# Kernel optimization log

Hardware: AMD Instinct MI355X
Metric: run time of the kernel (lower is better)

Reference implementation:

```python
import jax, jax.numpy as jnp
import numpy as np

B, T, D, V, L = 32, 512, 512, 1024, 128
BLANK = 0
NEG = -1e30  # log-domain 'minus infinity' that is fp-safe


def setup_inputs() -> dict:
    key = jax.random.key(0)
    k1, k2, k3 = jax.random.split(key, 3)
    x = jax.random.normal(k1, (B, T, D), dtype=jnp.float32)
    W = jax.random.normal(k2, (D, V), dtype=jnp.float32) / np.sqrt(D).astype(np.float32)
    b = jnp.zeros((V,), dtype=jnp.float32)
    # CTC targets must be in [1, V) (never the blank id 0)
    target = jax.random.randint(k3, (B, L), 1, V)
    input_lengths = jnp.full((B,), T, dtype=jnp.int32)
    target_lengths = jnp.full((B,), L, dtype=jnp.int32)
    return {"x": x, "W": W, "b": b, "target": target,
            "input_lengths": input_lengths, "target_lengths": target_lengths}


def _ctc_loss(log_probs, target, input_lengths, target_lengths):
    # log_probs: [T, B, V] (time-major), target: [B, L]
    Tt, Bb, _ = log_probs.shape
    Ll = target.shape[1]
    S = 2 * Ll + 1  # extended label sequence: blank,t0,blank,t1,...,blank
    ext = jnp.full((Bb, S), BLANK, dtype=target.dtype).at[:, 1::2].set(target)  # [B,S]
    ext_m2 = jnp.pad(ext, ((0, 0), (2, 0)), constant_values=BLANK)[:, :S]
    skip = (ext != BLANK) & (ext != ext_m2) & (jnp.arange(S)[None, :] >= 2)  # [B,S]

    # gather log-probs of extended labels for every time step: [T,B,S]
    lp_ext = jnp.take_along_axis(log_probs, jnp.broadcast_to(ext[None], (Tt, Bb, S)), axis=2)

    alpha0 = jnp.full((Bb, S), NEG, log_probs.dtype)
    alpha0 = alpha0.at[:, 0].set(lp_ext[0, :, 0]).at[:, 1].set(lp_ext[0, :, 1])

    def step(alpha, lp_t):
        a1 = jnp.pad(alpha, ((0, 0), (1, 0)), constant_values=NEG)[:, :S]
        a2 = jnp.pad(alpha, ((0, 0), (2, 0)), constant_values=NEG)[:, :S]
        c = jnp.logaddexp(alpha, a1)
        c = jnp.where(skip, jnp.logaddexp(c, a2), c)
        new = c + lp_t
        return new, new

    _, alphas = jax.lax.scan(step, alpha0, lp_ext[1:])
    alphas = jnp.concatenate([alpha0[None], alphas], axis=0)  # [T,B,S]

    bi = jnp.arange(Bb)
    a_last = alphas[input_lengths - 1, bi]  # [B,S] alpha at each sample's final frame
    ll = jnp.logaddexp(a_last[bi, 2 * target_lengths - 1], a_last[bi, 2 * target_lengths])
    nll = -ll  # per-sample negative log-likelihood
    # zero_infinity=True: infinite losses are zeroed
    nll = jnp.where(jnp.isinf(nll) | (nll > 1e29), 0.0, nll)
    # reduction='mean': divide each loss by its target length, then mean
    return jnp.mean(nll / jnp.maximum(target_lengths, 1).astype(nll.dtype))


def reference(x, W, b, target, input_lengths, target_lengths):
    logits = jnp.einsum('btd,dv->btv', x, W) + b  # nn.Linear
    log_probs = jax.nn.log_softmax(logits, axis=-1)  # [B,T,V]
    return _ctc_loss(jnp.transpose(log_probs, (1, 0, 2)), target, input_lengths, target_lengths)
```

## Files before the change

### kernel.cpp

```cpp
#include <hip/hip_runtime.h>
#include <cstdint>


#define SPAD 260
#define PEXT_PAD_ROWS 32
#define L2E 1.4426950408889634f
#define LN2 0.6931471805599453f

typedef short v8s __attribute__((ext_vector_type(8)));
typedef float v4f __attribute__((ext_vector_type(4)));

__device__ __forceinline__ uint32_t f2bf_bits(float f) {
  uint32_t u = __float_as_uint(f);
  return (u + 0x7FFFu + ((u >> 16) & 1u)) >> 16;
}
__device__ __forceinline__ float bf2f(uint32_t h) { return __uint_as_float(h << 16); }

__global__ void k_convert_x(const float* __restrict__ x, uint16_t* __restrict__ xb, long long n) {
  long long i = ((long long)blockIdx.x * blockDim.x + threadIdx.x) * 8;
  if (i >= n) return;
  float4 a = *(const float4*)(x + i);
  float4 b = *(const float4*)(x + i + 4);
  uint4 o;
  o.x = f2bf_bits(a.x) | (f2bf_bits(a.y) << 16);
  o.y = f2bf_bits(a.z) | (f2bf_bits(a.w) << 16);
  o.z = f2bf_bits(b.x) | (f2bf_bits(b.y) << 16);
  o.w = f2bf_bits(b.z) | (f2bf_bits(b.w) << 16);
  *(uint4*)(xb + i) = o;
}

__global__ void k_transpose_w(const float* __restrict__ W, uint16_t* __restrict__ Wt, int D, int V) {
  __shared__ float tile[32][33];
  int n0 = blockIdx.x * 32, k0 = blockIdx.y * 32;
  int tx = threadIdx.x, ty = threadIdx.y;
  #pragma unroll
  for (int i = 0; i < 32; i += 8)
    tile[ty + i][tx] = W[(size_t)(k0 + ty + i) * V + n0 + tx];
  __syncthreads();
  #pragma unroll
  for (int i = 0; i < 32; i += 8)
    Wt[(size_t)(n0 + ty + i) * D + k0 + tx] = (uint16_t)f2bf_bits(tile[tx][ty + i]);
}

template <typename CT>
__global__ __launch_bounds__(256) void k_gemm(const uint16_t* __restrict__ A,
                                              const uint16_t* __restrict__ Bt,
                                              const float* __restrict__ bias,
                                              CT* __restrict__ C, int M, int N, int K) {
  __shared__ uint16_t As[128 * 32];
  __shared__ uint16_t Bs[128 * 32];
  const int tid = threadIdx.x, lane = tid & 63, wave = tid >> 6;
  const int m0 = blockIdx.x * 128, n0 = blockIdx.y * 128;
  const int wm = wave & 1, wn = wave >> 1;
  const int frow = lane & 15, kb = lane >> 4;
  const int lr = lane >> 2, kc = lane & 3;
  v4f acc[4][4] = {};

  for (int k0 = 0; k0 < K; k0 += 32) {
    __syncthreads();
    #pragma unroll
    for (int i = 0; i < 2; i++) {
      const int r = (wave * 2 + i) * 16 + lr;
      const uint16_t* ga = A + (size_t)(m0 + r) * K + k0 + kc * 8;
      const uint16_t* gb = Bt + (size_t)(n0 + r) * K + k0 + kc * 8;
      __builtin_amdgcn_global_load_lds(
          (const __attribute__((address_space(1))) void*)ga,
          (__attribute__((address_space(3))) void*)(As + (wave * 2 + i) * 512 + lane * 8), 16, 0, 0);
      __builtin_amdgcn_global_load_lds(
          (const __attribute__((address_space(1))) void*)gb,
          (__attribute__((address_space(3))) void*)(Bs + (wave * 2 + i) * 512 + lane * 8), 16, 0, 0);
    }
    __syncthreads();

    v8s af[4], bf[4];
    #pragma unroll
    for (int i = 0; i < 4; i++)
      af[i] = *(const v8s*)(As + (wm * 64 + i * 16 + frow) * 32 + kb * 8);
    #pragma unroll
    for (int j = 0; j < 4; j++)
      bf[j] = *(const v8s*)(Bs + (wn * 64 + j * 16 + frow) * 32 + kb * 8);
    #pragma unroll
    for (int i = 0; i < 4; i++)
      #pragma unroll
      for (int j = 0; j < 4; j++)
        acc[i][j] = __builtin_amdgcn_mfma_f32_16x16x32_bf16(af[i], bf[j], acc[i][j], 0, 0, 0);
  }

  const int crow = (lane >> 4) * 4, ccol = lane & 15;
  #pragma unroll
  for (int j = 0; j < 4; j++) {
    const int n = n0 + wn * 64 + j * 16 + ccol;
    const float bv = bias[n];
    #pragma unroll
    for (int i = 0; i < 4; i++) {
      const int mb = m0 + wm * 64 + i * 16 + crow;
      #pragma unroll
      for (int r2 = 0; r2 < 4; r2++) {
        float v = acc[i][j][r2] + bv;
        if constexpr (sizeof(CT) == 2) C[(size_t)(mb + r2) * N + n] = (CT)f2bf_bits(v);
        else                           C[(size_t)(mb + r2) * N + n] = v;
      }
    }
  }
}

template <typename CT>
__global__ void k_softmax_gather(const CT* __restrict__ logits, const int* __restrict__ target,
                                 const int* __restrict__ tlen, float* __restrict__ pext,
                                 int T, int V, int L) {
  const int row = blockIdx.x * 4 + (threadIdx.x >> 6);
  const int lane = threadIdx.x & 63;
  const CT* lrow = logits + (size_t)row * V;

  float xs[16];
  int cnt = 0;
  float mx = -INFINITY;
  for (int base = 0; base < V; base += 256) {
    const int idx = base + lane * 4;
    float4 v;
    if constexpr (sizeof(CT) == 2) {
      uint2 u = *(const uint2*)((const uint16_t*)lrow + idx);
      v.x = bf2f(u.x & 0xFFFFu); v.y = bf2f(u.x >> 16);
      v.z = bf2f(u.y & 0xFFFFu); v.w = bf2f(u.y >> 16);
    } else {
      v = *(const float4*)((const float*)lrow + idx);
    }
    xs[cnt] = v.x; xs[cnt + 1] = v.y; xs[cnt + 2] = v.z; xs[cnt + 3] = v.w; cnt += 4;
    mx = fmaxf(mx, fmaxf(fmaxf(v.x, v.y), fmaxf(v.z, v.w)));
  }
  #pragma unroll
  for (int off = 32; off; off >>= 1) mx = fmaxf(mx, __shfl_xor(mx, off, 64));
  float sum = 0.f;
  #pragma unroll
  for (int q = 0; q < 16; q++) { if (q < cnt) sum += exp2f((xs[q] - mx) * L2E); }
  #pragma unroll
  for (int off = 32; off; off >>= 1) sum += __shfl_xor(sum, off, 64);
  const float lse2 = mx * L2E + log2f(sum);

  const int bidx = row / T;
  const int Lb = tlen[bidx];
  const int S = 2 * Lb + 1;
  float* prow = pext + (size_t)row * SPAD;
  for (int s = lane; s < SPAD; s += 64) {
    float p = 0.f;
    if (s < S) {
      const int lbl = (s & 1) ? target[bidx * L + ((s - 1) >> 1)] : 0;
      float lg;
      if constexpr (sizeof(CT) == 2) lg = bf2f(((const uint16_t*)lrow)[lbl]);
      else                           lg = ((const float*)lrow)[lbl];
      p = exp2f(lg * L2E - lse2);
    }
    prow[s] = p;
  }
}

__device__ __forceinline__ float wave_shr1(float x) {
  return __int_as_float(__builtin_amdgcn_update_dpp(0, __float_as_int(x), 0x138, 0xf, 0xf, true));
}
__device__ __forceinline__ float wave_max_nonneg(float x) {
  x = fmaxf(x, __int_as_float(__builtin_amdgcn_update_dpp(0, __float_as_int(x), 0x111, 0xf, 0xf, true)));
  x = fmaxf(x, __int_as_float(__builtin_amdgcn_update_dpp(0, __float_as_int(x), 0x112, 0xf, 0xf, true)));
  x = fmaxf(x, __int_as_float(__builtin_amdgcn_update_dpp(0, __float_as_int(x), 0x114, 0xf, 0xf, true)));
  x = fmaxf(x, __int_as_float(__builtin_amdgcn_update_dpp(0, __float_as_int(x), 0x118, 0xf, 0xf, true)));
  x = fmaxf(x, __int_as_float(__builtin_amdgcn_update_dpp(0, __float_as_int(x), 0x142, 0xf, 0xf, true)));
  x = fmaxf(x, __int_as_float(__builtin_amdgcn_update_dpp(0, __float_as_int(x), 0x143, 0xf, 0xf, true)));
  return __int_as_float(__builtin_amdgcn_readlane(__float_as_int(x), 63));
}

__device__ __forceinline__ void load16(float4* __restrict__ p, float* __restrict__ p4,
                                       const float* __restrict__ pb, int t0, int lane) {
  #pragma unroll
  for (int k = 0; k < 16; k++) {
    const float* row = pb + (size_t)(t0 + k) * SPAD;
    p[k] = *(const float4*)(row + (lane << 2));
    p4[k] = row[256];
  }
}

__global__ __launch_bounds__(64, 1) void k_ctc(const float* __restrict__ pext,
                                               const int* __restrict__ target,
                                               const int* __restrict__ ilen,
                                               const int* __restrict__ tlen,
                                               float* __restrict__ loss, int T, int L) {
  const int b = blockIdx.x;
  const int lane = threadIdx.x;
  const int Tb = ilen[b];
  const int Lb = tlen[b];
  const int S = 2 * Lb + 1;
  const int* tg = target + b * L;

  const int s1 = 4 * lane + 1, s3 = 4 * lane + 3;
  float sk1 = 0.f, sk3 = 0.f;
  if (s1 >= 3 && s1 < S) sk1 = (tg[(s1 - 1) >> 1] != tg[(s1 - 3) >> 1]) ? 1.f : 0.f;
  if (s3 >= 3 && s3 < S) sk3 = (tg[(s3 - 1) >> 1] != tg[(s3 - 3) >> 1]) ? 1.f : 0.f;

  const float* pb = pext + (size_t)b * T * SPAD;
  const float4 p0 = *(const float4*)(pb + (lane << 2));
  float a0 = (lane == 0) ? p0.x : 0.f;
  float a1 = (lane == 0) ? p0.y : 0.f;
  float a2 = 0.f, a3 = 0.f, a4 = 0.f;
  float log2C = 0.f;

  #define CTC_STEP(PP, P4) {                                            \
    const float pm3 = wave_shr1(a3);                                    \
    const float a255 = __int_as_float(__builtin_amdgcn_readlane(__float_as_int(a3), 63)); \
    const float n0v = (a0 + pm3) * (PP).x;                              \
    const float n1v = (a1 + a0 + sk1 * pm3) * (PP).y;                   \
    const float n2v = (a2 + a1) * (PP).z;                               \
    const float n3v = (a3 + a2 + sk3 * a1) * (PP).w;                    \
    const float n4v = (a4 + a255) * (P4);                               \
    a0 = n0v; a1 = n1v; a2 = n2v; a3 = n3v; a4 = n4v; }

  #define RENORM {                                                      \
    float m = fmaxf(fmaxf(fmaxf(a0, a1), fmaxf(a2, a3)), a4);           \
    m = wave_max_nonneg(m);                                             \
    const int e = (int)((__float_as_uint(m) >> 23) & 255u) - 127;       \
    const float scale = __uint_as_float((uint32_t)(127 - e) << 23);     \
    a0 *= scale; a1 *= scale; a2 *= scale; a3 *= scale; a4 *= scale;    \
    log2C += (float)e; }

  float4 pA[16], pB[16];
  float p4A[16], p4B[16];
  int t0 = 1;
  load16(pA, p4A, pb, t0, lane);

  while (t0 < Tb) {
    load16(pB, p4B, pb, t0 + 16, lane);
    #pragma unroll
    for (int k = 0; k < 16; k++) {
      if (t0 + k < Tb) CTC_STEP(pA[k], p4A[k]);
      if ((k & 7) == 7) RENORM;
    }
    t0 += 16;
    if (t0 >= Tb) break;
    load16(pA, p4A, pb, t0 + 16, lane);
    #pragma unroll
    for (int k = 0; k < 16; k++) {
      if (t0 + k < Tb) CTC_STEP(pB[k], p4B[k]);
      if ((k & 7) == 7) RENORM;
    }
    t0 += 16;
  }

  __shared__ float abuf[257];
  abuf[4 * lane + 0] = a0; abuf[4 * lane + 1] = a1;
  abuf[4 * lane + 2] = a2; abuf[4 * lane + 3] = a3;
  if (lane == 63) abuf[256] = a4;
  __syncthreads();
  if (lane == 0) {
    const float ssum = abuf[2 * Lb - 1] + abuf[2 * Lb];
    const float ll = (log2f(ssum) + log2C) * LN2;
    float nll = -ll;
    if (!(nll < 1e29f)) nll = 0.f;
    loss[b] = nll / (float)(Lb > 0 ? Lb : 1);
  }
}

__global__ void k_reduce(const float* __restrict__ loss, float* __restrict__ out, int B) {
  const int lane = threadIdx.x;
  float v = (lane < B) ? loss[lane] : 0.f;
  #pragma unroll
  for (int off = 32; off; off >>= 1) v += __shfl_xor(v, off, 64);
  if (lane == 0) out[0] = v / (float)B;
}

extern "C" void kernel_launch(void* const* d_in, const int* in_sizes, int n_in,
                              void* d_out, int out_size, void* d_ws, size_t ws_size,
                              hipStream_t stream) {
  const float* x      = (const float*)d_in[0];
  const float* W      = (const float*)d_in[1];
  const float* bias   = (const float*)d_in[2];
  const int*  target  = (const int*)d_in[3];
  const int*  ilen    = (const int*)d_in[4];
  const int*  tlen    = (const int*)d_in[5];

  const int B = in_sizes[4];
  const int V = in_sizes[2];
  const int D = in_sizes[1] / V;
  const int T = in_sizes[0] / (B * D);
  const int L = in_sizes[3] / B;
  const int M = B * T;

  char* ws = (char*)d_ws;
  const size_t xb_bytes = (size_t)M * D * 2;
  const size_t wt_bytes = (size_t)V * D * 2;
  const size_t pext_bytes = (size_t)(M + PEXT_PAD_ROWS) * SPAD * 4;
  uint16_t* xb = (uint16_t*)ws;
  uint16_t* Wt = (uint16_t*)(ws + xb_bytes);
  char* logits = ws + xb_bytes + wt_bytes;

  const size_t need_f32 = xb_bytes + wt_bytes + (size_t)M * V * 4 + 4096;
  const bool f32log = (ws_size >= need_f32);
  const size_t log_bytes = (size_t)M * V * (f32log ? 4 : 2);

  float* pext;
  size_t tail = xb_bytes + wt_bytes + log_bytes;
  if (pext_bytes <= xb_bytes + wt_bytes) {
    pext = (float*)ws;
  } else {
    pext = (float*)(ws + tail); tail += pext_bytes;
  }
  float* lossb = (float*)(ws + tail);

  const long long nx = (long long)M * D;
  k_convert_x<<<(int)((nx / 8 + 255) / 256), 256, 0, stream>>>(x, xb, nx);
  k_transpose_w<<<dim3(V / 32, D / 32), dim3(32, 8), 0, stream>>>(W, Wt, D, V);
  if (f32log) {
    float* lg = (float*)logits;
    k_gemm<float><<<dim3(M / 128, V / 128), 256, 0, stream>>>(xb, Wt, bias, lg, M, V, D);
    k_softmax_gather<float><<<M / 4, 256, 0, stream>>>(lg, target, tlen, pext, T, V, L);
  } else {
    uint16_t* lg = (uint16_t*)logits;
    k_gemm<uint16_t><<<dim3(M / 128, V / 128), 256, 0, stream>>>(xb, Wt, bias, lg, M, V, D);
    k_softmax_gather<uint16_t><<<M / 4, 256, 0, stream>>>(lg, target, tlen, pext, T, V, L);
  }
  k_ctc<<<B, 64, 0, stream>>>(pext, target, ilen, tlen, lossb, T, L);
  k_reduce<<<1, 64, 0, stream>>>(lossb, (float*)d_out, B);
}
```

Before: 177.0 us.

## Merge prep kernels, force bf16 logits, deepen CTC prefetch, atomic loss reduce

Merges the x conversion and W transpose into one launch that also zeroes the output, and drops the final reduce kernel by having each CTC block atomically add its scaled loss. Logits are always stored as bf16, which halves logit traffic between the GEMM and the softmax compared with the f32 path chosen when workspace allowed. The CTC recurrence now prefetches with a four-buffer ring of 8-step chunks instead of two 16-step buffers, keeping loads further ahead of use. The risks are lower logit precision and a nondeterministic float summation order from the atomics.

```diff
diff --git a/kernel.cpp b/kernel.cpp
--- a/kernel.cpp
+++ b/kernel.cpp
@@ -3,7 +3,7 @@
 
 
 #define SPAD 260
-#define PEXT_PAD_ROWS 32
+#define PEXT_PAD_ROWS 64
 #define L2E 1.4426950408889634f
 #define LN2 0.6931471805599453f
 
@@ -16,37 +16,40 @@
 }
 __device__ __forceinline__ float bf2f(uint32_t h) { return __uint_as_float(h << 16); }
 
-__global__ void k_convert_x(const float* __restrict__ x, uint16_t* __restrict__ xb, long long n) {
-  long long i = ((long long)blockIdx.x * blockDim.x + threadIdx.x) * 8;
-  if (i >= n) return;
-  float4 a = *(const float4*)(x + i);
-  float4 b = *(const float4*)(x + i + 4);
-  uint4 o;
-  o.x = f2bf_bits(a.x) | (f2bf_bits(a.y) << 16);
-  o.y = f2bf_bits(a.z) | (f2bf_bits(a.w) << 16);
-  o.z = f2bf_bits(b.x) | (f2bf_bits(b.y) << 16);
-  o.w = f2bf_bits(b.z) | (f2bf_bits(b.w) << 16);
-  *(uint4*)(xb + i) = o;
-}
-
-__global__ void k_transpose_w(const float* __restrict__ W, uint16_t* __restrict__ Wt, int D, int V) {
-  __shared__ float tile[32][33];
-  int n0 = blockIdx.x * 32, k0 = blockIdx.y * 32;
-  int tx = threadIdx.x, ty = threadIdx.y;
-  #pragma unroll
-  for (int i = 0; i < 32; i += 8)
-    tile[ty + i][tx] = W[(size_t)(k0 + ty + i) * V + n0 + tx];
-  __syncthreads();
-  #pragma unroll
-  for (int i = 0; i < 32; i += 8)
-    Wt[(size_t)(n0 + ty + i) * D + k0 + tx] = (uint16_t)f2bf_bits(tile[tx][ty + i]);
-}
-
-template <typename CT>
+__global__ void k_prep(const float* __restrict__ x, uint16_t* __restrict__ xb, long long n,
+                       const float* __restrict__ W, uint16_t* __restrict__ Wt, int D, int V,
+                       float* __restrict__ out, int nconv) {
+  if (blockIdx.x == 0 && threadIdx.x == 0) out[0] = 0.f;
+  if ((int)blockIdx.x < nconv) {
+    long long i = ((long long)blockIdx.x * blockDim.x + threadIdx.x) * 8;
+    if (i >= n) return;
+    float4 a = *(const float4*)(x + i);
+    float4 b = *(const float4*)(x + i + 4);
+    uint4 o;
+    o.x = f2bf_bits(a.x) | (f2bf_bits(a.y) << 16);
+    o.y = f2bf_bits(a.z) | (f2bf_bits(a.w) << 16);
+    o.z = f2bf_bits(b.x) | (f2bf_bits(b.y) << 16);
+    o.w = f2bf_bits(b.z) | (f2bf_bits(b.w) << 16);
+    *(uint4*)(xb + i) = o;
+  } else {
+    __shared__ float tile[32][33];
+    const int bid2 = blockIdx.x - nconv;
+    const int n0 = (bid2 % (V / 32)) * 32, k0 = (bid2 / (V / 32)) * 32;
+    const int tx = threadIdx.x & 31, ty = threadIdx.x >> 5;
+    #pragma unroll
+    for (int i = 0; i < 32; i += 8)
+      tile[ty + i][tx] = W[(size_t)(k0 + ty + i) * V + n0 + tx];
+    __syncthreads();
+    #pragma unroll
+    for (int i = 0; i < 32; i += 8)
+      Wt[(size_t)(n0 + ty + i) * D + k0 + tx] = (uint16_t)f2bf_bits(tile[tx][ty + i]);
+  }
+}
+
 __global__ __launch_bounds__(256) void k_gemm(const uint16_t* __restrict__ A,
                                               const uint16_t* __restrict__ Bt,
                                               const float* __restrict__ bias,
-                                              CT* __restrict__ C, int M, int N, int K) {
+                                              uint16_t* __restrict__ C, int M, int N, int K) {
   __shared__ uint16_t As[128 * 32];
   __shared__ uint16_t Bs[128 * 32];
   const int tid = threadIdx.x, lane = tid & 63, wave = tid >> 6;
@@ -95,36 +98,28 @@
     for (int i = 0; i < 4; i++) {
       const int mb = m0 + wm * 64 + i * 16 + crow;
       #pragma unroll
-      for (int r2 = 0; r2 < 4; r2++) {
-        float v = acc[i][j][r2] + bv;
-        if constexpr (sizeof(CT) == 2) C[(size_t)(mb + r2) * N + n] = (CT)f2bf_bits(v);
-        else                           C[(size_t)(mb + r2) * N + n] = v;
-      }
+      for (int r2 = 0; r2 < 4; r2++)
+        C[(size_t)(mb + r2) * N + n] = (uint16_t)f2bf_bits(acc[i][j][r2] + bv);
     }
   }
 }
 
-template <typename CT>
-__global__ void k_softmax_gather(const CT* __restrict__ logits, const int* __restrict__ target,
+__global__ void k_softmax_gather(const uint16_t* __restrict__ logits, const int* __restrict__ target,
                                  const int* __restrict__ tlen, float* __restrict__ pext,
                                  int T, int V, int L) {
   const int row = blockIdx.x * 4 + (threadIdx.x >> 6);
   const int lane = threadIdx.x & 63;
-  const CT* lrow = logits + (size_t)row * V;
+  const uint16_t* lrow = logits + (size_t)row * V;
 
   float xs[16];
   int cnt = 0;
   float mx = -INFINITY;
   for (int base = 0; base < V; base += 256) {
     const int idx = base + lane * 4;
+    uint2 u = *(const uint2*)(lrow + idx);
     float4 v;
-    if constexpr (sizeof(CT) == 2) {
-      uint2 u = *(const uint2*)((const uint16_t*)lrow + idx);
-      v.x = bf2f(u.x & 0xFFFFu); v.y = bf2f(u.x >> 16);
-      v.z = bf2f(u.y & 0xFFFFu); v.w = bf2f(u.y >> 16);
-    } else {
-      v = *(const float4*)((const float*)lrow + idx);
-    }
+    v.x = bf2f(u.x & 0xFFFFu); v.y = bf2f(u.x >> 16);
+    v.z = bf2f(u.y & 0xFFFFu); v.w = bf2f(u.y >> 16);
     xs[cnt] = v.x; xs[cnt + 1] = v.y; xs[cnt + 2] = v.z; xs[cnt + 3] = v.w; cnt += 4;
     mx = fmaxf(mx, fmaxf(fmaxf(v.x, v.y), fmaxf(v.z, v.w)));
   }
@@ -145,10 +140,7 @@
     float p = 0.f;
     if (s < S) {
       const int lbl = (s & 1) ? target[bidx * L + ((s - 1) >> 1)] : 0;
-      float lg;
-      if constexpr (sizeof(CT) == 2) lg = bf2f(((const uint16_t*)lrow)[lbl]);
-      else                           lg = ((const float*)lrow)[lbl];
-      p = exp2f(lg * L2E - lse2);
+      p = exp2f(bf2f(lrow[lbl]) * L2E - lse2);
     }
     prow[s] = p;
   }
@@ -167,10 +159,10 @@
   return __int_as_float(__builtin_amdgcn_readlane(__float_as_int(x), 63));
 }
 
-__device__ __forceinline__ void load16(float4* __restrict__ p, float* __restrict__ p4,
-                                       const float* __restrict__ pb, int t0, int lane) {
-  #pragma unroll
-  for (int k = 0; k < 16; k++) {
+__device__ __forceinline__ void load8(float4* __restrict__ p, float* __restrict__ p4,
+                                      const float* __restrict__ pb, int t0, int lane) {
+  #pragma unroll
+  for (int k = 0; k < 8; k++) {
     const float* row = pb + (size_t)(t0 + k) * SPAD;
     p[k] = *(const float4*)(row + (lane << 2));
     p4[k] = row[256];
@@ -181,9 +173,10 @@
                                                const int* __restrict__ target,
                                                const int* __restrict__ ilen,
                                                const int* __restrict__ tlen,
-                                               float* __restrict__ loss, int T, int L) {
+                                               float* __restrict__ out, int T, int L) {
   const int b = blockIdx.x;
   const int lane = threadIdx.x;
+  const int B = gridDim.x;
   const int Tb = ilen[b];
   const int Lb = tlen[b];
   const int S = 2 * Lb + 1;
@@ -219,27 +212,31 @@
     a0 *= scale; a1 *= scale; a2 *= scale; a3 *= scale; a4 *= scale;    \
     log2C += (float)e; }
 
-  float4 pA[16], pB[16];
-  float p4A[16], p4B[16];
+  float4 Pa[8], Pb_[8], Pc[8], Pd[8];
+  float Qa[8], Qb[8], Qc[8], Qd[8];
   int t0 = 1;
-  load16(pA, p4A, pb, t0, lane);
-
-  while (t0 < Tb) {
-    load16(pB, p4B, pb, t0 + 16, lane);
-    #pragma unroll
-    for (int k = 0; k < 16; k++) {
-      if (t0 + k < Tb) CTC_STEP(pA[k], p4A[k]);
-      if ((k & 7) == 7) RENORM;
-    }
-    t0 += 16;
-    if (t0 >= Tb) break;
-    load16(pA, p4A, pb, t0 + 16, lane);
-    #pragma unroll
-    for (int k = 0; k < 16; k++) {
-      if (t0 + k < Tb) CTC_STEP(pB[k], p4B[k]);
-      if ((k & 7) == 7) RENORM;
-    }
-    t0 += 16;
+  bool done = false;
+  load8(Pa, Qa, pb, t0, lane);
+  load8(Pb_, Qb, pb, t0 + 8, lane);
+  load8(Pc, Qc, pb, t0 + 16, lane);
+
+  #define PHASE(LP, LQ, CP, CQ) {                                       \
+    if (t0 + 8 <= Tb) {                                                 \
+      load8(LP, LQ, pb, t0 + 24, lane);                                 \
+      _Pragma("unroll")                                                 \
+      for (int k = 0; k < 8; k++) CTC_STEP(CP[k], CQ[k]);               \
+      RENORM; t0 += 8;                                                  \
+    } else {                                                            \
+      _Pragma("unroll")                                                 \
+      for (int k = 0; k < 8; k++) { if (t0 + k < Tb) CTC_STEP(CP[k], CQ[k]); } \
+      RENORM; done = true;                                              \
+    } }
+
+  while (!done) {
+    PHASE(Pd, Qd, Pa, Qa); if (done) break;
+    PHASE(Pa, Qa, Pb_, Qb); if (done) break;
+    PHASE(Pb_, Qb, Pc, Qc); if (done) break;
+    PHASE(Pc, Qc, Pd, Qd);
   }
 
   __shared__ float abuf[257];
@@ -252,16 +249,8 @@
     const float ll = (log2f(ssum) + log2C) * LN2;
     float nll = -ll;
     if (!(nll < 1e29f)) nll = 0.f;
-    loss[b] = nll / (float)(Lb > 0 ? Lb : 1);
-  }
-}
-
-__global__ void k_reduce(const float* __restrict__ loss, float* __restrict__ out, int B) {
-  const int lane = threadIdx.x;
-  float v = (lane < B) ? loss[lane] : 0.f;
-  #pragma unroll
-  for (int off = 32; off; off >>= 1) v += __shfl_xor(v, off, 64);
-  if (lane == 0) out[0] = v / (float)B;
+    atomicAdd(out, nll / ((float)(Lb > 0 ? Lb : 1) * (float)B));
+  }
 }
 
 extern "C" void kernel_launch(void* const* d_in, const int* in_sizes, int n_in,
@@ -287,33 +276,21 @@
   const size_t pext_bytes = (size_t)(M + PEXT_PAD_ROWS) * SPAD * 4;
   uint16_t* xb = (uint16_t*)ws;
   uint16_t* Wt = (uint16_t*)(ws + xb_bytes);
-  char* logits = ws + xb_bytes + wt_bytes;
-
-  const size_t need_f32 = xb_bytes + wt_bytes + (size_t)M * V * 4 + 4096;
-  const bool f32log = (ws_size >= need_f32);
-  const size_t log_bytes = (size_t)M * V * (f32log ? 4 : 2);
+  uint16_t* logits = (uint16_t*)(ws + xb_bytes + wt_bytes);
+  const size_t log_bytes = (size_t)M * V * 2;
 
   float* pext;
-  size_t tail = xb_bytes + wt_bytes + log_bytes;
   if (pext_bytes <= xb_bytes + wt_bytes) {
     pext = (float*)ws;
   } else {
-    pext = (float*)(ws + tail); tail += pext_bytes;
-  }
-  float* lossb = (float*)(ws + tail);
+    pext = (float*)(ws + xb_bytes + wt_bytes + log_bytes);
+  }
 
   const long long nx = (long long)M * D;
-  k_convert_x<<<(int)((nx / 8 + 255) / 256), 256, 0, stream>>>(x, xb, nx);
-  k_transpose_w<<<dim3(V / 32, D / 32), dim3(32, 8), 0, stream>>>(W, Wt, D, V);
-  if (f32log) {
-    float* lg = (float*)logits;
-    k_gemm<float><<<dim3(M / 128, V / 128), 256, 0, stream>>>(xb, Wt, bias, lg, M, V, D);
-    k_softmax_gather<float><<<M / 4, 256, 0, stream>>>(lg, target, tlen, pext, T, V, L);
-  } else {
-    uint16_t* lg = (uint16_t*)logits;
-    k_gemm<uint16_t><<<dim3(M / 128, V / 128), 256, 0, stream>>>(xb, Wt, bias, lg, M, V, D);
-    k_softmax_gather<uint16_t><<<M / 4, 256, 0, stream>>>(lg, target, tlen, pext, T, V, L);
-  }
-  k_ctc<<<B, 64, 0, stream>>>(pext, target, ilen, tlen, lossb, T, L);
-  k_reduce<<<1, 64, 0, stream>>>(lossb, (float*)d_out, B);
-}
+  const int nconv = (int)((nx / 8 + 255) / 256);
+  const int ntrans = (V / 32) * (D / 32);
+  k_prep<<<nconv + ntrans, 256, 0, stream>>>(x, xb, nx, W, Wt, D, V, (float*)d_out, nconv);
+  k_gemm<<<dim3(M / 128, V / 128), 256, 0, stream>>>(xb, Wt, bias, logits, M, V, D);
+  k_softmax_gather<<<M / 4, 256, 0, stream>>>(logits, target, tlen, pext, T, V, L);
+  k_ctc<<<B, 64, 0, stream>>>(pext, target, ilen, tlen, (float*)d_out, T, L);
+}
```

Result: faster. 169.9 us (-4.0%).
